# Optimization experiments

Measured on AMD Instinct MI355X. Metric: run time of the kernel, lower is better.

Reference implementation:

```python
import jax, jax.numpy as jnp
import numpy as np
import math

H_HEADS, N_LEVELS, N_POINTS, DIM = 8, 4, 4, 256
HEAD_DIM = DIM // H_HEADS
SHAPES = np.array([[150, 150], [75, 75], [38, 38], [19, 19]], dtype=np.int32)
LEVEL_START = np.concatenate([[0], np.cumsum(SHAPES[:, 0] * SHAPES[:, 1])[:-1]]).astype(np.int32)
NUM_VALUE = int((SHAPES[:, 0] * SHAPES[:, 1]).sum())  # 29930
BS, NQ = 4, 22500


def _offset_bias():
    # Deformable-DETR init: points arranged on rays per head
    thetas = np.arange(H_HEADS, dtype=np.float32) * (2.0 * math.pi / H_HEADS)
    grid = np.stack([np.cos(thetas), np.sin(thetas)], -1)
    grid = grid / np.abs(grid).max(-1, keepdims=True)
    grid = np.tile(grid[:, None, None, :], (1, N_LEVELS, N_POINTS, 1))
    grid = grid * (np.arange(N_POINTS, dtype=np.float32) + 1.0)[None, None, :, None]
    return jnp.asarray(grid.reshape(-1))


def setup_inputs() -> dict:
    key = jax.random.key(0)
    ks = jax.random.split(key, 8)
    xav = lambda k, fi, fo: jax.random.normal(k, (fi, fo), jnp.float32) * np.float32(math.sqrt(2.0 / (fi + fo)))
    return {
        "query": jax.random.normal(ks[0], (BS, NQ, DIM), jnp.float32),
        "value": jax.random.normal(ks[1], (BS, NUM_VALUE, DIM), jnp.float32),
        "reference_points": jax.random.uniform(ks[2], (BS, NQ, N_LEVELS, 2), jnp.float32),
        "spatial_shapes": jnp.asarray(SHAPES),
        "level_start_index": jnp.asarray(LEVEL_START),
        "W_so": xav(ks[3], DIM, H_HEADS * N_LEVELS * N_POINTS * 2) * 0.1,
        "b_so": _offset_bias(),
        "W_aw": xav(ks[4], DIM, H_HEADS * N_LEVELS * N_POINTS) * 0.1,
        "b_aw": jnp.zeros((H_HEADS * N_LEVELS * N_POINTS,), jnp.float32),
        "W_v": xav(ks[5], DIM, DIM),
        "b_v": jnp.zeros((DIM,), jnp.float32),
        "W_o": xav(ks[6], DIM, DIM),
        "b_o": jnp.zeros((DIM,), jnp.float32),
    }


def _sample_level(v_l, loc_l, h, w):
    # v_l: (bs, H, h*w, hd); loc_l: (bs, nq, H, P, 2) in [0,1] normalized coords
    # torch grid_sample bilinear, align_corners=False, padding_mode='zeros'
    bs, nq = loc_l.shape[0], loc_l.shape[1]
    x = jnp.transpose(loc_l[..., 0], (0, 2, 1, 3)).reshape(bs, H_HEADS, nq * N_POINTS) * w - 0.5
    y = jnp.transpose(loc_l[..., 1], (0, 2, 1, 3)).reshape(bs, H_HEADS, nq * N_POINTS) * h - 0.5
    x0 = jnp.floor(x); y0 = jnp.floor(y)
    lx = x - x0; ly = y - y0

    def gather(xi, yi, wgt):
        valid = ((xi >= 0) & (xi < w) & (yi >= 0) & (yi < h)).astype(v_l.dtype)
        idx = (jnp.clip(yi, 0, h - 1) * w + jnp.clip(xi, 0, w - 1)).astype(jnp.int32)
        g = jnp.take_along_axis(v_l, idx[..., None], axis=2)  # (bs,H,nq*P,hd)
        return g * (wgt * valid)[..., None]

    x0i = x0.astype(jnp.int32); y0i = y0.astype(jnp.int32)
    out = (gather(x0i, y0i, (1 - lx) * (1 - ly))
           + gather(x0i + 1, y0i, lx * (1 - ly))
           + gather(x0i, y0i + 1, (1 - lx) * ly)
           + gather(x0i + 1, y0i + 1, lx * ly))
    return out.reshape(bs, H_HEADS, nq, N_POINTS, HEAD_DIM)


def reference(query, value, reference_points, spatial_shapes, level_start_index,
              W_so, b_so, W_aw, b_aw, W_v, b_v, W_o, b_o):
    shapes = np.asarray(jax.device_get(spatial_shapes))  # static level shapes
    starts = np.asarray(jax.device_get(level_start_index))
    bs, nq, _ = query.shape
    nv = value.shape[1]

    v = (value @ W_v + b_v).reshape(bs, nv, H_HEADS, HEAD_DIM)
    v = jnp.transpose(v, (0, 2, 1, 3))  # (bs, H, nv, hd)

    off = (query @ W_so + b_so).reshape(bs, nq, H_HEADS, N_LEVELS, N_POINTS, 2)
    aw = jax.nn.softmax((query @ W_aw + b_aw).reshape(bs, nq, H_HEADS, N_LEVELS * N_POINTS), axis=-1)
    aw = aw.reshape(bs, nq, H_HEADS, N_LEVELS, N_POINTS)

    norm = jnp.asarray(np.stack([shapes[:, 1], shapes[:, 0]], -1), query.dtype)  # (L, 2) = (W, H)
    loc = reference_points[:, :, None, :, None, :] + off / norm[None, None, None, :, None, :]

    res = jnp.zeros((bs, nq, H_HEADS, HEAD_DIM), query.dtype)
    for lvl in range(N_LEVELS):
        h, w = int(shapes[lvl, 0]), int(shapes[lvl, 1])
        s = int(starts[lvl])
        v_l = v[:, :, s:s + h * w, :]
        sampled = _sample_level(v_l, loc[:, :, :, lvl], h, w)  # (bs,H,nq,P,hd)
        res = res + jnp.einsum('bhqpd,bqhp->bqhd', sampled, aw[:, :, :, lvl])

    out = res.reshape(bs, nq, DIM) @ W_o + b_o
    return out  # dropout is identity in eval mode
```

## Files before the change

### kernel.cpp

```cpp
#include <hip/hip_runtime.h>
#include <hip/hip_bf16.h>

#define HH 8
#define NL 4
#define NP 4
#define DDIM 256
#define HD 32
#define BSZ 4
#define NQQ 22500
#define NVV 29930

typedef __attribute__((ext_vector_type(4))) float f32x4;
typedef __attribute__((ext_vector_type(2))) float f32x2;
typedef __attribute__((ext_vector_type(8))) short s16x8;
typedef __attribute__((ext_vector_type(4))) unsigned int u32x4;

__device__ __forceinline__ unsigned int cvtpk(float lo, float hi) {
    unsigned int r;
    asm("v_cvt_pk_bf16_f32 %0, %1, %2" : "=v"(r) : "v"(lo), "v"(hi));
    return r;
}
__device__ __forceinline__ unsigned int cvtpk1(float lo) {
    unsigned int r;
    asm("v_cvt_pk_bf16_f32 %0, %1, 0" : "=v"(r) : "v"(lo));
    return r;
}
__device__ __forceinline__ unsigned short bfb(float x) {
    union { float f; unsigned int i; } u; u.f = x;
    unsigned int lsb = (u.i >> 16) & 1u;
    u.i += 0x7fffu + lsb;
    return (unsigned short)(u.i >> 16);
}
__device__ __forceinline__ s16x8 cvt8(f32x4 a, f32x4 b) {
    union { unsigned int u[4]; s16x8 v; } r;
    r.u[0] = cvtpk(a[0], a[1]);
    r.u[1] = cvtpk(a[2], a[3]);
    r.u[2] = cvtpk(b[0], b[1]);
    r.u[3] = cvtpk(b[2], b[3]);
    return r.v;
}
__device__ __forceinline__ void pk_fma(f32x2& a, f32x2 v, f32x2 w) {
    asm("v_pk_fma_f32 %0, %1, %2, %0" : "+v"(a) : "v"(v), "v"(w));
}

__global__ __launch_bounds__(64) void k_pack(
    const float* __restrict__ Wso, const float* __restrict__ Waw,
    const float* __restrict__ Wv,  const float* __restrict__ Wo,
    unsigned short* __restrict__ pWv, unsigned short* __restrict__ pQP,
    unsigned short* __restrict__ pWo)
{
    const int ctg = blockIdx.x;
    const int lane = threadIdx.x;
    const float* src; unsigned short* dst; int N, col, ct;
    if (ctg < 16)      { ct = ctg;      dst = pWv; src = Wv; N = 256; col = ct*16 + (lane&15); }
    else if (ctg < 40) { ct = ctg - 16; dst = pQP;
        if (ct < 16) { src = Wso; N = 256; col = ct*16 + (lane&15); }
        else         { src = Waw; N = 128; col = (ct-16)*16 + (lane&15); } }
    else               { ct = ctg - 40; dst = pWo; src = Wo; N = 256; col = ct*16 + (lane&15); }

    for (int ks = 0; ks < 8; ++ks) {
        const int k0 = ks*32 + (lane>>4)*8;
        unsigned short tmp[8];
#pragma unroll
        for (int i = 0; i < 8; ++i) tmp[i] = bfb(src[(size_t)(k0 + i) * N + col]);
        unsigned short* d = dst + ((size_t)(ct*8 + ks)*64 + lane)*8;
#pragma unroll
        for (int i = 0; i < 8; ++i) d[i] = tmp[i];
    }
}

__global__ __launch_bounds__(256) void k_value_proj(
    const float* __restrict__ value,
    const float* __restrict__ bv,
    const unsigned short* __restrict__ pWv,
    unsigned short* __restrict__ vout)
{
    const int tid = threadIdx.x;
    const int b   = blockIdx.y;
    const int row0 = blockIdx.x * 64;
    const int w = tid >> 6, lane = tid & 63;
    const int mrow = lane & 15, kg = lane >> 4;

    const int rowa = row0 + w*16 + mrow;
    const bool rv = rowa < NVV;
    const float* ap = value + ((size_t)b * NVV + (rv ? rowa : 0)) * DDIM + kg*8;

    s16x8 af[8];
#pragma unroll
    for (int ks = 0; ks < 8; ++ks) {
        f32x4 a0 = {0.f,0.f,0.f,0.f}, a1 = a0;
        if (rv) {
            a0 = __builtin_nontemporal_load((const f32x4*)(ap + ks*32));
            a1 = __builtin_nontemporal_load((const f32x4*)(ap + ks*32 + 4));
        }
        af[ks] = cvt8(a0, a1);
    }
    const s16x8* bp = (const s16x8*)pWv;
#pragma unroll 2
    for (int ct = 0; ct < 16; ++ct) {
        const float bias = bv[ct*16 + mrow];
        f32x4 acc = {bias, bias, bias, bias};
#pragma unroll
        for (int ks = 0; ks < 8; ++ks)
            acc = __builtin_amdgcn_mfma_f32_16x16x32_bf16(af[ks], bp[(ct*8 + ks)*64 + lane], acc, 0, 0, 0);
        const int h = ct >> 1, d = (ct & 1)*16 + mrow;
        unsigned short* vp = vout + ((size_t)(b*HH + h) * NVV) * HD + d;
#pragma unroll
        for (int r = 0; r < 4; ++r) {
            const int rowd = row0 + w*16 + kg*4 + r;
            if (rowd < NVV) vp[(size_t)rowd * HD] = (unsigned short)cvtpk1(acc[r]);
        }
    }
}

__global__ __launch_bounds__(256, 5) void k_query_fused(
    const float* __restrict__ query,
    const float* __restrict__ refpt,
    const unsigned short* __restrict__ pQP,
    const unsigned short* __restrict__ pWo,
    const float* __restrict__ bso, const float* __restrict__ baw,
    const float* __restrict__ bo,
    const unsigned short* __restrict__ v,
    float* __restrict__ out)
{
    __shared__ __align__(16) unsigned char s_a8[16 * 512];
    __shared__ float s_so[8 * 512];
    __shared__ float s_aw[8 * 256];

    const int tid = threadIdx.x;
    const int b   = blockIdx.y;
    const int q0  = blockIdx.x * 16;
    const int w = tid >> 6, lane = tid & 63;
    const int mrow = lane & 15, kg = lane >> 4;

    {
        const int r  = tid >> 4;
        const int c0 = (tid & 15) * 16;
        const bool rv = (q0 + r) < NQQ;
        const float* qrow = query + ((size_t)b * NQQ + q0 + r) * DDIM + c0;
        f32x4 a0 = {0,0,0,0}, a1 = a0, a2 = a0, a3 = a0;
        if (rv) {
            a0 = __builtin_nontemporal_load((const f32x4*)(qrow));
            a1 = __builtin_nontemporal_load((const f32x4*)(qrow+4));
            a2 = __builtin_nontemporal_load((const f32x4*)(qrow+8));
            a3 = __builtin_nontemporal_load((const f32x4*)(qrow+12));
        }
        const int base = r*512 + c0*2;
        const int sw = (r & 7) << 4;
        *(s16x8*)(s_a8 + ((base     ) ^ sw)) = cvt8(a0, a1);
        *(s16x8*)(s_a8 + ((base + 16) ^ sw)) = cvt8(a2, a3);
    }
    __syncthreads();

    {
        s16x8 af[8];
        const int swz = (mrow & 7) << 4;
#pragma unroll
        for (int ks = 0; ks < 8; ++ks)
            af[ks] = *(const s16x8*)(s_a8 + ((mrow*512 + (ks*32 + kg*8)*2) ^ swz));
        const s16x8* bq = (const s16x8*)pQP;
#pragma unroll
        for (int t = 0; t < 6; ++t) {
            const int ct = w*6 + t;
            const float bias = (ct < 16) ? bso[ct*16 + mrow] : baw[(ct-16)*16 + mrow];
            f32x4 acc = {bias, bias, bias, bias};
#pragma unroll
            for (int ks = 0; ks < 8; ++ks)
                acc = __builtin_amdgcn_mfma_f32_16x16x32_bf16(af[ks], bq[(ct*8 + ks)*64 + lane], acc, 0, 0, 0);
            if (ct < 16) {
                const int c = ct*16 + mrow;
                float* d = s_so + (c >> 5)*512 + (c & 31)*16 + kg*4;
#pragma unroll
                for (int r = 0; r < 4; ++r) d[r] = acc[r];
            } else {
                const int c = (ct-16)*16 + mrow;
                float* d = s_aw + (c >> 4)*256 + (c & 15)*16 + kg*4;
#pragma unroll
                for (int r = 0; r < 4; ++r) d[r] = acc[r];
            }
        }
    }
    __syncthreads();

    if (tid < 128) {
        const int q = tid >> 3, h = tid & 7;
        float* p = s_aw + h * 256 + q;
        float m = p[0];
#pragma unroll
        for (int i = 1; i < 16; ++i) m = fmaxf(m, p[i*16]);
        float e[16], s = 0.f;
#pragma unroll
        for (int i = 0; i < 16; ++i) { e[i] = __expf(p[i*16] - m); s += e[i]; }
        const float inv = 1.f / s;
#pragma unroll
        for (int i = 0; i < 16; ++i) p[i*16] = e[i] * inv;
    }
    __syncthreads();

    {
        const int qs = lane >> 2;
        const int dg = lane & 3;
        const int qv = (q0 + qs < NQQ) ? (q0 + qs) : (NQQ - 1);
        const float2* rp2 = (const float2*)(refpt + ((size_t)b * NQQ + qv) * (NL * 2));
#pragma unroll
        for (int pass = 0; pass < 2; ++pass) {
            const int h = __builtin_amdgcn_readfirstlane(pass * 4 + w);
            const unsigned short* vbh = v + ((size_t)(b*HH + h) * NVV) * HD + dg*8;
            const float* soh = s_so + h * 512 + qs;
            const float* awh = s_aw + h * 256 + qs;
            f32x2 acc0 = {0.f,0.f}, acc1 = {0.f,0.f}, acc2 = {0.f,0.f}, acc3 = {0.f,0.f};
            const int hs_[4] = {150, 75, 38, 19};
            const int st_[4] = {0, 22500, 28125, 29569};
#pragma unroll
            for (int l = 0; l < NL; ++l) {
                const int L = hs_[l];
                const float Lf = (float)L;
                const float2 rxy = rp2[l];
                const unsigned short* vlp = vbh + (size_t)st_[l] * HD;
#pragma unroll
                for (int p = 0; p < NP; ++p) {
                    const int lp = l*4 + p;
                    const float ox  = soh[(2*lp    ) * 16];
                    const float oy  = soh[(2*lp + 1) * 16];
                    const float awv = awh[lp * 16];
                    const float x = fmaf(rxy.x, Lf, ox) - 0.5f;
                    const float y = fmaf(rxy.y, Lf, oy) - 0.5f;
                    const float xf = floorf(x), yf = floorf(y);
                    const float lx = x - xf, ly = y - yf;
                    const int x0 = (int)xf, y0 = (int)yf;
                    const int x1 = x0 + 1, y1 = y0 + 1;
                    const int cx0 = min(max(x0, 0), L-1), cx1 = min(max(x1, 0), L-1);
                    const int cy0 = min(max(y0, 0), L-1), cy1 = min(max(y1, 0), L-1);
                    const bool bx0 = (unsigned)x0 < (unsigned)L;
                    const bool bx1 = (unsigned)x1 < (unsigned)L;
                    const bool by0 = (unsigned)y0 < (unsigned)L;
                    const bool by1 = (unsigned)y1 < (unsigned)L;
                    const unsigned r0 = (unsigned)(cy0 * L), r1 = (unsigned)(cy1 * L);
                    const u32x4 c00 = *(const u32x4*)(vlp + (size_t)((r0 + cx0) * HD));
                    const u32x4 c10 = *(const u32x4*)(vlp + (size_t)((r0 + cx1) * HD));
                    const u32x4 c01 = *(const u32x4*)(vlp + (size_t)((r1 + cx0) * HD));
                    const u32x4 c11 = *(const u32x4*)(vlp + (size_t)((r1 + cx1) * HD));
                    const float t1 = awv * ly, t0 = awv - t1;
                    const float lxc = 1.f - lx;
                    const float w00 = (bx0 & by0) ? lxc * t0 : 0.f;
                    const float w10 = (bx1 & by0) ? lx  * t0 : 0.f;
                    const float w01 = (bx0 & by1) ? lxc * t1 : 0.f;
                    const float w11 = (bx1 & by1) ? lx  * t1 : 0.f;
#define CORNER(cv, wgt) { \
    f32x2 ww = {wgt, wgt}; \
    f32x2 v0 = {__uint_as_float((cv)[0] << 16), __uint_as_float((cv)[0] & 0xffff0000u)}; \
    f32x2 v1 = {__uint_as_float((cv)[1] << 16), __uint_as_float((cv)[1] & 0xffff0000u)}; \
    f32x2 v2 = {__uint_as_float((cv)[2] << 16), __uint_as_float((cv)[2] & 0xffff0000u)}; \
    f32x2 v3 = {__uint_as_float((cv)[3] << 16), __uint_as_float((cv)[3] & 0xffff0000u)}; \
    pk_fma(acc0, v0, ww); pk_fma(acc1, v1, ww); \
    pk_fma(acc2, v2, ww); pk_fma(acc3, v3, ww); }
                    CORNER(c00, w00)
                    CORNER(c10, w10)
                    CORNER(c01, w01)
                    CORNER(c11, w11)
#undef CORNER
                }
            }
            u32x4 rb;
            rb[0] = cvtpk(acc0[0], acc0[1]);
            rb[1] = cvtpk(acc1[0], acc1[1]);
            rb[2] = cvtpk(acc2[0], acc2[1]);
            rb[3] = cvtpk(acc3[0], acc3[1]);
            const int boff = qs*512 + (h*32 + dg*8)*2;
            *(u32x4*)(s_a8 + (boff ^ ((qs & 7) << 4))) = rb;
        }
    }
    __syncthreads();

    {
        s16x8 of[8];
        const int swz = (mrow & 7) << 4;
#pragma unroll
        for (int ks = 0; ks < 8; ++ks)
            of[ks] = *(const s16x8*)(s_a8 + ((mrow*512 + (ks*32 + kg*8)*2) ^ swz));
        const s16x8* bp = (const s16x8*)pWo;
#pragma unroll
        for (int t = 0; t < 4; ++t) {
            const int ct = w*4 + t;
            const float bias = bo[ct*16 + mrow];
            f32x4 acc = {bias, bias, bias, bias};
#pragma unroll
            for (int ks = 0; ks < 8; ++ks)
                acc = __builtin_amdgcn_mfma_f32_16x16x32_bf16(of[ks], bp[(ct*8 + ks)*64 + lane], acc, 0, 0, 0);
#pragma unroll
            for (int r = 0; r < 4; ++r) {
                const int q = kg*4 + r;
                if (q0 + q < NQQ)
                    __builtin_nontemporal_store(acc[r],
                        &out[((size_t)b * NQQ + q0 + q) * DDIM + ct*16 + mrow]);
            }
        }
    }
}

extern "C" void kernel_launch(void* const* d_in, const int* in_sizes, int n_in,
                              void* d_out, int out_size, void* d_ws, size_t ws_size,
                              hipStream_t stream) {
    const float* query = (const float*)d_in[0];
    const float* value = (const float*)d_in[1];
    const float* refpt = (const float*)d_in[2];
    const float* Wso = (const float*)d_in[5];
    const float* bso = (const float*)d_in[6];
    const float* Waw = (const float*)d_in[7];
    const float* baw = (const float*)d_in[8];
    const float* Wv  = (const float*)d_in[9];
    const float* bv  = (const float*)d_in[10];
    const float* Wo  = (const float*)d_in[11];
    const float* bo  = (const float*)d_in[12];
    float* out = (float*)d_out;

    unsigned short* v   = (unsigned short*)d_ws;
    unsigned short* pWv = (unsigned short*)((char*)d_ws + 61296640);
    unsigned short* pQP = pWv + 65536;
    unsigned short* pWo = pQP + 98304;

    k_pack<<<56, 64, 0, stream>>>(Wso, Waw, Wv, Wo, pWv, pQP, pWo);

    dim3 g1((NVV + 63) / 64, BSZ);
    k_value_proj<<<g1, 256, 0, stream>>>(value, bv, pWv, v);

    dim3 g2((NQQ + 15) / 16, BSZ);
    k_query_fused<<<g2, 256, 0, stream>>>(query, refpt, pQP, pWo, bso, baw, bo, v, out);
}
```

Before: 353.3 us.

## Switch intermediates to fp16 and accumulate bilinear sampling with packed f16 FMA

Replaces bf16 storage and MFMA with fp16 throughout: weights, projected values and sampled features are stored as half, and the MFMAs use the f16 variant. Bilinear sampling now accumulates directly in packed fp16 with v_pk_fma_f16, which removes the bf16-to-fp32 unpacking and repacking around each corner. Shared offset and weight arrays are padded to a stride of 17 to reduce bank conflicts, and the occupancy hint drops from 5 to 4 blocks. The trade-off is fp16 accumulation across 64 weighted corner samples, which adds rounding error and overflow risk when values are large.

```diff
diff --git a/kernel.cpp b/kernel.cpp
--- a/kernel.cpp
+++ b/kernel.cpp
@@ -1,5 +1,5 @@
 #include <hip/hip_runtime.h>
-#include <hip/hip_bf16.h>
+#include <hip/hip_fp16.h>
 
 #define HH 8
 #define NL 4
@@ -11,36 +11,25 @@
 #define NVV 29930
 
 typedef __attribute__((ext_vector_type(4))) float f32x4;
-typedef __attribute__((ext_vector_type(2))) float f32x2;
 typedef __attribute__((ext_vector_type(8))) short s16x8;
 typedef __attribute__((ext_vector_type(4))) unsigned int u32x4;
-
-__device__ __forceinline__ unsigned int cvtpk(float lo, float hi) {
-    unsigned int r;
-    asm("v_cvt_pk_bf16_f32 %0, %1, %2" : "=v"(r) : "v"(lo), "v"(hi));
-    return r;
-}
-__device__ __forceinline__ unsigned int cvtpk1(float lo) {
-    unsigned int r;
-    asm("v_cvt_pk_bf16_f32 %0, %1, 0" : "=v"(r) : "v"(lo));
-    return r;
-}
-__device__ __forceinline__ unsigned short bfb(float x) {
-    union { float f; unsigned int i; } u; u.f = x;
-    unsigned int lsb = (u.i >> 16) & 1u;
-    u.i += 0x7fffu + lsb;
-    return (unsigned short)(u.i >> 16);
-}
+typedef __attribute__((ext_vector_type(2))) __fp16 f16x2;
+
 __device__ __forceinline__ s16x8 cvt8(f32x4 a, f32x4 b) {
-    union { unsigned int u[4]; s16x8 v; } r;
-    r.u[0] = cvtpk(a[0], a[1]);
-    r.u[1] = cvtpk(a[2], a[3]);
-    r.u[2] = cvtpk(b[0], b[1]);
-    r.u[3] = cvtpk(b[2], b[3]);
+    union { f16x2 h[4]; s16x8 v; } r;
+    r.h[0] = __builtin_amdgcn_cvt_pkrtz(a[0], a[1]);
+    r.h[1] = __builtin_amdgcn_cvt_pkrtz(a[2], a[3]);
+    r.h[2] = __builtin_amdgcn_cvt_pkrtz(b[0], b[1]);
+    r.h[3] = __builtin_amdgcn_cvt_pkrtz(b[2], b[3]);
     return r.v;
 }
-__device__ __forceinline__ void pk_fma(f32x2& a, f32x2 v, f32x2 w) {
-    asm("v_pk_fma_f32 %0, %1, %2, %0" : "+v"(a) : "v"(v), "v"(w));
+__device__ __forceinline__ unsigned int wpair(float w) {
+    union { f16x2 h; unsigned int u; } x;
+    x.h = __builtin_amdgcn_cvt_pkrtz(w, w);
+    return x.u;
+}
+__device__ __forceinline__ void pkfma16(unsigned int& acc, unsigned int v, unsigned int w) {
+    asm("v_pk_fma_f16 %0, %1, %2, %0" : "+v"(acc) : "v"(v), "v"(w));
 }
 
 __global__ __launch_bounds__(64) void k_pack(
@@ -62,7 +51,8 @@
         const int k0 = ks*32 + (lane>>4)*8;
         unsigned short tmp[8];
 #pragma unroll
-        for (int i = 0; i < 8; ++i) tmp[i] = bfb(src[(size_t)(k0 + i) * N + col]);
+        for (int i = 0; i < 8; ++i)
+            tmp[i] = __half_as_ushort(__float2half(src[(size_t)(k0 + i) * N + col]));
         unsigned short* d = dst + ((size_t)(ct*8 + ks)*64 + lane)*8;
 #pragma unroll
         for (int i = 0; i < 8; ++i) d[i] = tmp[i];
@@ -102,18 +92,18 @@
         f32x4 acc = {bias, bias, bias, bias};
 #pragma unroll
         for (int ks = 0; ks < 8; ++ks)
-            acc = __builtin_amdgcn_mfma_f32_16x16x32_bf16(af[ks], bp[(ct*8 + ks)*64 + lane], acc, 0, 0, 0);
+            acc = __builtin_amdgcn_mfma_f32_16x16x32_f16(af[ks], bp[(ct*8 + ks)*64 + lane], acc, 0, 0, 0);
         const int h = ct >> 1, d = (ct & 1)*16 + mrow;
         unsigned short* vp = vout + ((size_t)(b*HH + h) * NVV) * HD + d;
 #pragma unroll
         for (int r = 0; r < 4; ++r) {
             const int rowd = row0 + w*16 + kg*4 + r;
-            if (rowd < NVV) vp[(size_t)rowd * HD] = (unsigned short)cvtpk1(acc[r]);
-        }
-    }
-}
-
-__global__ __launch_bounds__(256, 5) void k_query_fused(
+            if (rowd < NVV) vp[(size_t)rowd * HD] = __half_as_ushort(__float2half(acc[r]));
+        }
+    }
+}
+
+__global__ __launch_bounds__(256, 4) void k_query_fused(
     const float* __restrict__ query,
     const float* __restrict__ refpt,
     const unsigned short* __restrict__ pQP,
@@ -124,8 +114,8 @@
     float* __restrict__ out)
 {
     __shared__ __align__(16) unsigned char s_a8[16 * 512];
-    __shared__ float s_so[8 * 512];
-    __shared__ float s_aw[8 * 256];
+    __shared__ float s_so[8 * 544];
+    __shared__ float s_aw[8 * 272];
 
     const int tid = threadIdx.x;
     const int b   = blockIdx.y;
@@ -166,15 +156,15 @@
             f32x4 acc = {bias, bias, bias, bias};
 #pragma unroll
             for (int ks = 0; ks < 8; ++ks)
-                acc = __builtin_amdgcn_mfma_f32_16x16x32_bf16(af[ks], bq[(ct*8 + ks)*64 + lane], acc, 0, 0, 0);
+                acc = __builtin_amdgcn_mfma_f32_16x16x32_f16(af[ks], bq[(ct*8 + ks)*64 + lane], acc, 0, 0, 0);
             if (ct < 16) {
                 const int c = ct*16 + mrow;
-                float* d = s_so + (c >> 5)*512 + (c & 31)*16 + kg*4;
+                float* d = s_so + (c >> 5)*544 + (c & 31)*17 + kg*4;
 #pragma unroll
                 for (int r = 0; r < 4; ++r) d[r] = acc[r];
             } else {
                 const int c = (ct-16)*16 + mrow;
-                float* d = s_aw + (c >> 4)*256 + (c & 15)*16 + kg*4;
+                float* d = s_aw + (c >> 4)*272 + (c & 15)*17 + kg*4;
 #pragma unroll
                 for (int r = 0; r < 4; ++r) d[r] = acc[r];
             }
@@ -183,17 +173,17 @@
     __syncthreads();
 
     if (tid < 128) {
-        const int q = tid >> 3, h = tid & 7;
-        float* p = s_aw + h * 256 + q;
+        const int q = tid & 15, h = tid >> 4;
+        float* p = s_aw + h * 272 + q;
         float m = p[0];
 #pragma unroll
-        for (int i = 1; i < 16; ++i) m = fmaxf(m, p[i*16]);
+        for (int i = 1; i < 16; ++i) m = fmaxf(m, p[i*17]);
         float e[16], s = 0.f;
 #pragma unroll
-        for (int i = 0; i < 16; ++i) { e[i] = __expf(p[i*16] - m); s += e[i]; }
+        for (int i = 0; i < 16; ++i) { e[i] = __expf(p[i*17] - m); s += e[i]; }
         const float inv = 1.f / s;
 #pragma unroll
-        for (int i = 0; i < 16; ++i) p[i*16] = e[i] * inv;
+        for (int i = 0; i < 16; ++i) p[i*17] = e[i] * inv;
     }
     __syncthreads();
 
@@ -206,9 +196,9 @@
         for (int pass = 0; pass < 2; ++pass) {
             const int h = __builtin_amdgcn_readfirstlane(pass * 4 + w);
             const unsigned short* vbh = v + ((size_t)(b*HH + h) * NVV) * HD + dg*8;
-            const float* soh = s_so + h * 512 + qs;
-            const float* awh = s_aw + h * 256 + qs;
-            f32x2 acc0 = {0.f,0.f}, acc1 = {0.f,0.f}, acc2 = {0.f,0.f}, acc3 = {0.f,0.f};
+            const float* soh = s_so + h * 544 + qs;
+            const float* awh = s_aw + h * 272 + qs;
+            unsigned int acc0 = 0, acc1 = 0, acc2 = 0, acc3 = 0;
             const int hs_[4] = {150, 75, 38, 19};
             const int st_[4] = {0, 22500, 28125, 29569};
 #pragma unroll
@@ -220,9 +210,9 @@
 #pragma unroll
                 for (int p = 0; p < NP; ++p) {
                     const int lp = l*4 + p;
-                    const float ox  = soh[(2*lp    ) * 16];
-                    const float oy  = soh[(2*lp + 1) * 16];
-                    const float awv = awh[lp * 16];
+                    const float ox  = soh[(2*lp    ) * 17];
+                    const float oy  = soh[(2*lp + 1) * 17];
+                    const float awv = awh[lp * 17];
                     const float x = fmaf(rxy.x, Lf, ox) - 0.5f;
                     const float y = fmaf(rxy.y, Lf, oy) - 0.5f;
                     const float xf = floorf(x), yf = floorf(y);
@@ -247,13 +237,9 @@
                     const float w01 = (bx0 & by1) ? lxc * t1 : 0.f;
                     const float w11 = (bx1 & by1) ? lx  * t1 : 0.f;
 #define CORNER(cv, wgt) { \
-    f32x2 ww = {wgt, wgt}; \
-    f32x2 v0 = {__uint_as_float((cv)[0] << 16), __uint_as_float((cv)[0] & 0xffff0000u)}; \
-    f32x2 v1 = {__uint_as_float((cv)[1] << 16), __uint_as_float((cv)[1] & 0xffff0000u)}; \
-    f32x2 v2 = {__uint_as_float((cv)[2] << 16), __uint_as_float((cv)[2] & 0xffff0000u)}; \
-    f32x2 v3 = {__uint_as_float((cv)[3] << 16), __uint_as_float((cv)[3] & 0xffff0000u)}; \
-    pk_fma(acc0, v0, ww); pk_fma(acc1, v1, ww); \
-    pk_fma(acc2, v2, ww); pk_fma(acc3, v3, ww); }
+    const unsigned int wp_ = wpair(wgt); \
+    pkfma16(acc0, (cv)[0], wp_); pkfma16(acc1, (cv)[1], wp_); \
+    pkfma16(acc2, (cv)[2], wp_); pkfma16(acc3, (cv)[3], wp_); }
                     CORNER(c00, w00)
                     CORNER(c10, w10)
                     CORNER(c01, w01)
@@ -261,11 +247,7 @@
 #undef CORNER
                 }
             }
-            u32x4 rb;
-            rb[0] = cvtpk(acc0[0], acc0[1]);
-            rb[1] = cvtpk(acc1[0], acc1[1]);
-            rb[2] = cvtpk(acc2[0], acc2[1]);
-            rb[3] = cvtpk(acc3[0], acc3[1]);
+            u32x4 rb = {acc0, acc1, acc2, acc3};
             const int boff = qs*512 + (h*32 + dg*8)*2;
             *(u32x4*)(s_a8 + (boff ^ ((qs & 7) << 4))) = rb;
         }
@@ -286,7 +268,7 @@
             f32x4 acc = {bias, bias, bias, bias};
 #pragma unroll
             for (int ks = 0; ks < 8; ++ks)
-                acc = __builtin_amdgcn_mfma_f32_16x16x32_bf16(of[ks], bp[(ct*8 + ks)*64 + lane], acc, 0, 0, 0);
+                acc = __builtin_amdgcn_mfma_f32_16x16x32_f16(of[ks], bp[(ct*8 + ks)*64 + lane], acc, 0, 0, 0);
 #pragma unroll
             for (int r = 0; r < 4; ++r) {
                 const int q = kg*4 + r;
```

New measurement: 349.7 us. About the same (-1.0%).
